# Optimization experiments

Measured on AMD Instinct MI355X. Metric: run time of the kernel, lower is better.

## Reference

```python
import jax, jax.numpy as jnp
from jax import lax
import numpy as np

D_MODEL, D_STATE, EXPAND, D_CONV = 1024, 16, 2, 4
D_INNER = EXPAND * D_MODEL
B, L = 4, 2048


def setup_inputs() -> dict:
    key = jax.random.key(0)
    ks = jax.random.split(key, 12)
    def xavier(k, shape):
        fan_in, fan_out = shape[1], shape[0]
        lim = float(np.sqrt(6.0 / (fan_in + fan_out)))
        return jax.random.uniform(k, shape, jnp.float32, -lim, lim)
    inp = {}
    inp['x'] = jax.random.normal(ks[0], (B, L, D_MODEL), jnp.float32)
    inp['W_left'] = xavier(ks[1], (D_INNER, D_MODEL))
    inp['conv_w'] = jax.random.normal(ks[2], (D_INNER, 1, D_CONV), jnp.float32) * (1.0 / np.sqrt(D_CONV))
    inp['conv_b'] = jax.random.normal(ks[3], (D_INNER,), jnp.float32) * 0.01
    inp['W_delta'] = jax.random.normal(ks[4], (D_INNER, D_INNER), jnp.float32) * (1.0 / np.sqrt(D_INNER))
    inp['b_delta'] = jnp.zeros((D_INNER,), jnp.float32)
    inp['W_B'] = jax.random.normal(ks[5], (D_STATE, D_INNER), jnp.float32) * (1.0 / np.sqrt(D_INNER))
    inp['W_C'] = jax.random.normal(ks[6], (D_STATE, D_INNER), jnp.float32) * (1.0 / np.sqrt(D_INNER))
    inp['A_log'] = jnp.log(jnp.arange(1, D_STATE + 1, dtype=jnp.float32))
    inp['W_right'] = xavier(ks[7], (D_INNER, D_MODEL))
    inp['ln_g'] = jnp.ones((D_INNER,), jnp.float32)
    inp['ln_b'] = jnp.zeros((D_INNER,), jnp.float32)
    inp['W_out'] = xavier(ks[8], (D_MODEL, D_INNER))
    return inp


def _ssm(xl, W_delta, b_delta, W_B, W_C, A_log):
    # xl: [b, l, d_inner]
    b, l, d_inner = xl.shape
    A = -jax.nn.softplus(A_log)  # [d_state]
    delta = jnp.clip(jax.nn.softplus(xl @ W_delta.T + b_delta), 1e-4, 10.0)
    Bm = xl @ W_B.T  # [b, l, d_state]
    Cm = xl @ W_C.T  # [b, l, d_state]

    def step(h, inp):
        d_t, x_t, B_t, C_t = inp  # [b,d_inner], [b,d_inner], [b,N], [b,N]
        A_bar = jnp.exp(d_t[:, :, None] * A)            # [b, d_inner, N]
        h = A_bar * h + (d_t * x_t)[:, :, None] * B_t[:, None, :]
        y_t = jnp.einsum('bdn,bn->bd', h, C_t)
        return h, y_t

    h0 = jnp.zeros((b, d_inner, A_log.shape[0]), xl.dtype)
    xs = (jnp.swapaxes(delta, 0, 1), jnp.swapaxes(xl, 0, 1),
          jnp.swapaxes(Bm, 0, 1), jnp.swapaxes(Cm, 0, 1))
    _, ys = lax.scan(step, h0, xs)  # ys: [l, b, d_inner]
    return jnp.swapaxes(ys, 0, 1)


def reference(x, W_left, conv_w, conv_b, W_delta, b_delta, W_B, W_C, A_log,
              W_right, ln_g, ln_b, W_out):
    d_conv = conv_w.shape[-1]
    # left branch: linear -> causal depthwise conv1d -> silu
    left = x @ W_left.T                          # [b, l, d_inner]
    left_ncw = jnp.swapaxes(left, 1, 2)          # [b, d_inner, l]
    left_ncw = jnp.pad(left_ncw, ((0, 0), (0, 0), (d_conv - 1, 0)))
    left_ncw = lax.conv_general_dilated(
        left_ncw, conv_w, window_strides=(1,), padding='VALID',
        feature_group_count=conv_w.shape[0]) + conv_b[None, :, None]
    left = jax.nn.silu(jnp.swapaxes(left_ncw, 1, 2))
    # selective scan
    ssm_out = _ssm(left, W_delta, b_delta, W_B, W_C, A_log)
    # right gate (eval mode: dropout off)
    gate = jax.nn.silu(x @ W_right.T)
    out = ssm_out * gate
    # layernorm over d_inner
    mu = jnp.mean(out, axis=-1, keepdims=True)
    var = jnp.mean(jnp.square(out - mu), axis=-1, keepdims=True)
    out = (out - mu) * lax.rsqrt(var + 1e-5) * ln_g + ln_b
    return out @ W_out.T
```

## Files before the change

### kernel.cpp

```cpp
#include <hip/hip_runtime.h>
#include <cstddef>

#define LL 2048
#define TOK 8192
#define DM 1024
#define DI 2048
#define NS 16

typedef _Float16 half_t;
typedef __attribute__((ext_vector_type(8))) _Float16 f16x8;
typedef __attribute__((ext_vector_type(4))) _Float16 f16x4;
typedef __attribute__((ext_vector_type(4))) float f32x4;

__device__ __forceinline__ float softplus_f(float x) {
  return fmaxf(x, 0.f) + log1pf(__expf(-fabsf(x)));
}
__device__ __forceinline__ float silu_f(float x) {
  return x / (1.f + __expf(-x));
}
__device__ __forceinline__ void gload_lds16(const void* g, void* l) {
  __builtin_amdgcn_global_load_lds((const __attribute__((address_space(1))) void*)g,
                                   (__attribute__((address_space(3))) void*)l, 16, 0, 0);
}
#define DPP_ADD(v, ctrl) \
  ((v) + __int_as_float(__builtin_amdgcn_update_dpp(0, __float_as_int(v), (ctrl), 0xf, 0xf, true)))

__device__ float g_buf[120881152];

__global__ __launch_bounds__(256) void f2h_k(const float* __restrict__ in,
                                             half_t* __restrict__ out, int n4) {
  const int i = blockIdx.x * 256 + threadIdx.x;
  if (i >= n4) return;
  const float4 v = ((const float4*)in)[i];
  f16x4 o;
  o[0] = (half_t)v.x; o[1] = (half_t)v.y; o[2] = (half_t)v.z; o[3] = (half_t)v.w;
  ((f16x4*)out)[i] = o;
}

__global__ __launch_bounds__(256) void zh_k(half_t* __restrict__ out, int n4) {
  const int i = blockIdx.x * 256 + threadIdx.x;
  if (i >= n4) return;
  f16x4 o;
  o[0] = (half_t)0.f; o[1] = (half_t)0.f; o[2] = (half_t)0.f; o[3] = (half_t)0.f;
  ((f16x4*)out)[i] = o;
}

template <int ACT>
__global__ __launch_bounds__(256) void gemm_mfma(const half_t* __restrict__ A,
                                                 const half_t* __restrict__ W,
                                                 const float* __restrict__ bias,
                                                 float* __restrict__ C,
                                                 int M, int N, int K) {
  __shared__ half_t lA[4096];
  __shared__ half_t lB[4096];
  const int tid = threadIdx.x;
  const int bm0 = blockIdx.y * 128, bn0 = blockIdx.x * 128;
  const int lane = tid & 63, wave = tid >> 6;
  const int q = lane >> 4, mr = lane & 15;
  const int wm = (wave >> 1) * 64, wn = (wave & 1) * 64;
  const int flat0 = tid, flat1 = tid + 256;
  const int kc0 = flat0 >> 7, r0 = flat0 & 127;
  const int kc1 = flat1 >> 7, r1 = flat1 & 127;

  f32x4 acc[4][4];
#pragma unroll
  for (int i = 0; i < 4; ++i)
#pragma unroll
    for (int j = 0; j < 4; ++j) acc[i][j] = (f32x4){0.f, 0.f, 0.f, 0.f};

  for (int k0 = 0; k0 < K; k0 += 32) {
    gload_lds16(A + (size_t)(bm0 + r0) * K + k0 + kc0 * 8, lA + (size_t)flat0 * 8);
    gload_lds16(A + (size_t)(bm0 + r1) * K + k0 + kc1 * 8, lA + (size_t)flat1 * 8);
    gload_lds16(W + (size_t)(bn0 + r0) * K + k0 + kc0 * 8, lB + (size_t)flat0 * 8);
    gload_lds16(W + (size_t)(bn0 + r1) * K + k0 + kc1 * 8, lB + (size_t)flat1 * 8);
    __syncthreads();
    f16x8 af[4], bg[4];
#pragma unroll
    for (int t = 0; t < 4; ++t) {
      af[t] = *(const f16x8*)(lA + ((q << 10) + ((wm + t * 16 + mr) << 3)));
      bg[t] = *(const f16x8*)(lB + ((q << 10) + ((wn + t * 16 + mr) << 3)));
    }
#pragma unroll
    for (int i = 0; i < 4; ++i)
#pragma unroll
      for (int j = 0; j < 4; ++j)
        acc[i][j] = __builtin_amdgcn_mfma_f32_16x16x32_f16(af[i], bg[j], acc[i][j], 0, 0, 0);
    __syncthreads();
  }

#pragma unroll
  for (int i = 0; i < 4; ++i) {
#pragma unroll
    for (int j = 0; j < 4; ++j) {
      const int col = bn0 + wn + j * 16 + mr;
      const float bv = bias ? bias[col] : 0.f;
#pragma unroll
      for (int r = 0; r < 4; ++r) {
        const int row = bm0 + wm + i * 16 + q * 4 + r;
        float v = acc[i][j][r] + bv;
        if (ACT == 1) v = silu_f(v);
        C[(size_t)row * N + col] = v;
      }
    }
  }
}

__global__ __launch_bounds__(256) void gemm_mfma_lg(const half_t* __restrict__ A,
                                                    const half_t* __restrict__ W,
                                                    float* __restrict__ left,
                                                    half_t* __restrict__ gateh) {
  __shared__ half_t lA[4096];
  __shared__ half_t lB[4096];
  const int tid = threadIdx.x;
  const int bm0 = blockIdx.y * 128, bn0 = blockIdx.x * 128;
  const int K = DM;
  const int lane = tid & 63, wave = tid >> 6;
  const int q = lane >> 4, mr = lane & 15;
  const int wm = (wave >> 1) * 64, wn = (wave & 1) * 64;
  const int flat1 = tid + 256;
  const int kc0 = tid >> 7, r0 = tid & 127;
  const int kc1 = flat1 >> 7, r1 = flat1 & 127;

  f32x4 acc[4][4];
#pragma unroll
  for (int i = 0; i < 4; ++i)
#pragma unroll
    for (int j = 0; j < 4; ++j) acc[i][j] = (f32x4){0.f, 0.f, 0.f, 0.f};

  for (int k0 = 0; k0 < K; k0 += 32) {
    gload_lds16(A + (size_t)(bm0 + r0) * K + k0 + kc0 * 8, lA + (size_t)tid * 8);
    gload_lds16(A + (size_t)(bm0 + r1) * K + k0 + kc1 * 8, lA + (size_t)flat1 * 8);
    gload_lds16(W + (size_t)(bn0 + r0) * K + k0 + kc0 * 8, lB + (size_t)tid * 8);
    gload_lds16(W + (size_t)(bn0 + r1) * K + k0 + kc1 * 8, lB + (size_t)flat1 * 8);
    __syncthreads();
    f16x8 af[4], bg[4];
#pragma unroll
    for (int t = 0; t < 4; ++t) {
      af[t] = *(const f16x8*)(lA + ((q << 10) + ((wm + t * 16 + mr) << 3)));
      bg[t] = *(const f16x8*)(lB + ((q << 10) + ((wn + t * 16 + mr) << 3)));
    }
#pragma unroll
    for (int i = 0; i < 4; ++i)
#pragma unroll
      for (int j = 0; j < 4; ++j)
        acc[i][j] = __builtin_amdgcn_mfma_f32_16x16x32_f16(af[i], bg[j], acc[i][j], 0, 0, 0);
    __syncthreads();
  }

  const int is_gate = (bn0 >= DI);
  const int cb = bn0 - (is_gate ? DI : 0);
  if (!is_gate) {
#pragma unroll
    for (int i = 0; i < 4; ++i)
#pragma unroll
      for (int j = 0; j < 4; ++j) {
        const int col = cb + wn + j * 16 + mr;
#pragma unroll
        for (int r = 0; r < 4; ++r) {
          const int row = bm0 + wm + i * 16 + q * 4 + r;
          left[(size_t)row * DI + col] = acc[i][j][r];
        }
      }
  } else {
#pragma unroll
    for (int i = 0; i < 4; ++i)
#pragma unroll
      for (int j = 0; j < 4; ++j) {
        const int col = cb + wn + j * 16 + mr;
#pragma unroll
        for (int r = 0; r < 4; ++r) {
          const int row = bm0 + wm + i * 16 + q * 4 + r;
          gateh[(size_t)row * DI + col] = (half_t)silu_f(acc[i][j][r]);
        }
      }
  }
}

__global__ __launch_bounds__(512, 4) void gemm_delta_bc(const half_t* __restrict__ A,
                                                        const half_t* __restrict__ W,
                                                        const float* __restrict__ bias,
                                                        half_t* __restrict__ dlth,
                                                        float* __restrict__ bcout) {
  __shared__ half_t lA[8192];
  __shared__ half_t lB[4096];
  const int tid = threadIdx.x;
  const int bm0 = blockIdx.y * 256, bn0 = blockIdx.x * 128;
  const int K = DI;
  const int lane = tid & 63, wave = tid >> 6;
  const int q = lane >> 4, mr = lane & 15;
  const int wm = (wave >> 1) * 64, wn = (wave & 1) * 64;
  const int aflat1 = tid + 512;
  const int akc0 = tid >> 8, ar0 = tid & 255;
  const int akc1 = aflat1 >> 8, ar1 = aflat1 & 255;
  const int wkc = tid >> 7, wr = tid & 127;

  f32x4 acc[4][4];
#pragma unroll
  for (int i = 0; i < 4; ++i)
#pragma unroll
    for (int j = 0; j < 4; ++j) acc[i][j] = (f32x4){0.f, 0.f, 0.f, 0.f};

  for (int k0 = 0; k0 < K; k0 += 32) {
    gload_lds16(A + (size_t)(bm0 + ar0) * K + k0 + akc0 * 8, lA + (size_t)tid * 8);
    gload_lds16(A + (size_t)(bm0 + ar1) * K + k0 + akc1 * 8, lA + (size_t)aflat1 * 8);
    gload_lds16(W + (size_t)(bn0 + wr) * K + k0 + wkc * 8, lB + (size_t)tid * 8);
    __syncthreads();
    f16x8 ah[4], bg[4];
#pragma unroll
    for (int t = 0; t < 4; ++t) {
      const int ao = (q << 11) + ((wm + t * 16 + mr) << 3);
      const int bo = (q << 10) + ((wn + t * 16 + mr) << 3);
      ah[t] = *(const f16x8*)(lA + ao);
      bg[t] = *(const f16x8*)(lB + bo);
    }
    __builtin_amdgcn_s_setprio(1);
#pragma unroll
    for (int i = 0; i < 4; ++i)
#pragma unroll
      for (int j = 0; j < 4; ++j)
        acc[i][j] = __builtin_amdgcn_mfma_f32_16x16x32_f16(ah[i], bg[j], acc[i][j], 0, 0, 0);
    __builtin_amdgcn_s_setprio(0);
    __syncthreads();
  }

  if (bn0 < DI) {
#pragma unroll
    for (int i = 0; i < 4; ++i) {
#pragma unroll
      for (int j = 0; j < 4; ++j) {
        const int col = bn0 + wn + j * 16 + mr;
        const float bv = bias[col];
#pragma unroll
        for (int r = 0; r < 4; ++r) {
          const int row = bm0 + wm + i * 16 + q * 4 + r;
          float v = softplus_f(acc[i][j][r] + bv);
          v = fminf(fmaxf(v, 1e-4f), 10.f);
          dlth[(size_t)row * DI + col] = (half_t)v;
        }
      }
    }
  } else {
#pragma unroll
    for (int i = 0; i < 4; ++i) {
#pragma unroll
      for (int j = 0; j < 4; ++j) {
        const int c = wn + j * 16 + mr;
        if (c < 32) {
          const int slot = (c < 16) ? (2 * c) : (2 * (c - 16) + 1);
#pragma unroll
          for (int r = 0; r < 4; ++r) {
            const int row = bm0 + wm + i * 16 + q * 4 + r;
            bcout[(size_t)row * 32 + slot] = acc[i][j][r];
          }
        }
      }
    }
  }
}

__global__ __launch_bounds__(256) void conv_silu_k(const float* __restrict__ left,
                                                   const float* __restrict__ cw,
                                                   const float* __restrict__ cb,
                                                   half_t* __restrict__ xch) {
  const int idx = blockIdx.x * 256 + threadIdx.x;
  const int d = idx & (DI - 1);
  const int bt = idx >> 11;
  const int t = bt & (LL - 1);
  const float4 wv = *(const float4*)(cw + (size_t)d * 4);
  float acc = cb[d];
  const size_t base = (size_t)idx;
  if (t >= 3) {
    acc += left[base - 3 * DI] * wv.x + left[base - 2 * DI] * wv.y +
           left[base - DI] * wv.z + left[base] * wv.w;
  } else {
    acc += left[base] * wv.w;
    if (t >= 1) acc += left[base - DI] * wv.z;
    if (t >= 2) acc += left[base - 2 * DI] * wv.y;
  }
  xch[base] = (half_t)silu_f(acc);
}

#define ST 32
__global__ __launch_bounds__(256) void scan_k(const half_t* __restrict__ dlth,
                                              const half_t* __restrict__ xch,
                                              const half_t* __restrict__ gateh,
                                              const float* __restrict__ bcp,
                                              const float* __restrict__ A_log,
                                              float* __restrict__ y) {
  __shared__ float dx2[16 * 68];
  __shared__ float bcs[ST * 32];
  __shared__ float ys[ST * 16];
  const int tid = threadIdx.x;
  const int b  = blockIdx.x >> 7;
  const int d0 = (blockIdx.x & 127) << 4;
  const int n  = tid & 15;
  const int ch = tid >> 4;
  const float An = -softplus_f(A_log[n]);

  const int t_a = tid >> 4, c_a = tid & 15;
  const int t_b = t_a + 16;

  float h = 0.f;
  const size_t batch_base = (size_t)b * LL * DI + d0;
  const size_t batch_bc   = (size_t)b * LL * 32;

  size_t rb_cur = batch_base;
  float g0, g1;
  {
    const size_t ra = rb_cur + (size_t)t_a * DI + c_a;
    const size_t rbx = rb_cur + (size_t)t_b * DI + c_a;
    const float d0v = (float)dlth[ra], x0v = (float)xch[ra];
    const float d1v = (float)dlth[rbx], x1v = (float)xch[rbx];
    g0 = (float)gateh[ra]; g1 = (float)gateh[rbx];
    const float2 b0 = *(const float2*)&bcp[batch_bc + (size_t)t_a * 32 + 2 * c_a];
    const float2 b1 = *(const float2*)&bcp[batch_bc + (size_t)t_b * 32 + 2 * c_a];
    *(float2*)&dx2[c_a * 68 + t_a * 2] = make_float2(d0v, x0v);
    *(float2*)&dx2[c_a * 68 + t_b * 2] = make_float2(d1v, x1v);
    *(float2*)&bcs[t_a * 32 + 2 * c_a] = b0;
    *(float2*)&bcs[t_b * 32 + 2 * c_a] = b1;
  }
  __syncthreads();

  for (int it = 0; it < LL / ST; ++it) {
    float nd0, nx0, ng0, nd1, nx1, ng1;
    float2 nb0, nb1;
    const size_t rb_nxt = batch_base + (size_t)(it + 1) * ST * DI;
    if (it + 1 < LL / ST) {
      const size_t ra = rb_nxt + (size_t)t_a * DI + c_a;
      const size_t rbx = rb_nxt + (size_t)t_b * DI + c_a;
      nd0 = (float)dlth[ra]; nx0 = (float)xch[ra]; ng0 = (float)gateh[ra];
      nd1 = (float)dlth[rbx]; nx1 = (float)xch[rbx]; ng1 = (float)gateh[rbx];
      const size_t bcb = batch_bc + (size_t)(it + 1) * ST * 32;
      nb0 = *(const float2*)&bcp[bcb + (size_t)t_a * 32 + 2 * c_a];
      nb1 = *(const float2*)&bcp[bcb + (size_t)t_b * 32 + 2 * c_a];
    }

    const float* dxp = &dx2[ch * 68];
#pragma unroll
    for (int tt = 0; tt < ST; tt += 2) {
      const float4 v = *(const float4*)&dxp[tt * 2];
      const float2 bc0 = *(const float2*)&bcs[tt * 32 + 2 * n];
      const float2 bc1 = *(const float2*)&bcs[(tt + 1) * 32 + 2 * n];
      float ab = __expf(v.x * An);
      h = fmaf(ab, h, v.x * v.y * bc0.x);
      float p = h * bc0.y;
      p = DPP_ADD(p, 0x111); p = DPP_ADD(p, 0x112);
      p = DPP_ADD(p, 0x114); p = DPP_ADD(p, 0x118);
      if (n == 15) ys[tt * 16 + ch] = p;
      ab = __expf(v.z * An);
      h = fmaf(ab, h, v.z * v.w * bc1.x);
      p = h * bc1.y;
      p = DPP_ADD(p, 0x111); p = DPP_ADD(p, 0x112);
      p = DPP_ADD(p, 0x114); p = DPP_ADD(p, 0x118);
      if (n == 15) ys[(tt + 1) * 16 + ch] = p;
    }
    __syncthreads();

    if (it + 1 < LL / ST) {
      *(float2*)&dx2[c_a * 68 + t_a * 2] = make_float2(nd0, nx0);
      *(float2*)&dx2[c_a * 68 + t_b * 2] = make_float2(nd1, nx1);
      *(float2*)&bcs[t_a * 32 + 2 * c_a] = nb0;
      *(float2*)&bcs[t_b * 32 + 2 * c_a] = nb1;
    }
    y[rb_cur + (size_t)t_a * DI + c_a] = ys[t_a * 16 + c_a] * g0;
    y[rb_cur + (size_t)t_b * DI + c_a] = ys[t_b * 16 + c_a] * g1;
    g0 = ng0; g1 = ng1;
    rb_cur = rb_nxt;
    __syncthreads();
  }
}

__global__ __launch_bounds__(256) void ln_k(const float* __restrict__ y,
                                            const float* __restrict__ gam,
                                            const float* __restrict__ bet,
                                            half_t* __restrict__ outn) {
  const int row = blockIdx.x;
  const int tid = threadIdx.x;
  const float* yr = y + (size_t)row * DI;
  const float4 v0 = ((const float4*)yr)[tid];
  const float4 v1 = ((const float4*)yr)[tid + 256];
  float s = v0.x + v0.y + v0.z + v0.w + v1.x + v1.y + v1.z + v1.w;
  float q = v0.x * v0.x + v0.y * v0.y + v0.z * v0.z + v0.w * v0.w +
            v1.x * v1.x + v1.y * v1.y + v1.z * v1.z + v1.w * v1.w;
  for (int off = 32; off > 0; off >>= 1) {
    s += __shfl_down(s, off);
    q += __shfl_down(q, off);
  }
  __shared__ float sred[4], qred[4];
  const int wid = tid >> 6;
  if ((tid & 63) == 0) { sred[wid] = s; qred[wid] = q; }
  __syncthreads();
  s = sred[0] + sred[1] + sred[2] + sred[3];
  q = qred[0] + qred[1] + qred[2] + qred[3];
  const float mu = s * (1.f / DI);
  const float rs = rsqrtf(q * (1.f / DI) - mu * mu + 1e-5f);
  half_t* orow = outn + (size_t)row * DI;
  const int c0 = tid * 4, c1 = (tid + 256) * 4;
  f16x4 o;
  o[0] = (half_t)((v0.x - mu) * rs * gam[c0 + 0] + bet[c0 + 0]);
  o[1] = (half_t)((v0.y - mu) * rs * gam[c0 + 1] + bet[c0 + 1]);
  o[2] = (half_t)((v0.z - mu) * rs * gam[c0 + 2] + bet[c0 + 2]);
  o[3] = (half_t)((v0.w - mu) * rs * gam[c0 + 3] + bet[c0 + 3]);
  ((f16x4*)orow)[tid] = o;
  o[0] = (half_t)((v1.x - mu) * rs * gam[c1 + 0] + bet[c1 + 0]);
  o[1] = (half_t)((v1.y - mu) * rs * gam[c1 + 1] + bet[c1 + 1]);
  o[2] = (half_t)((v1.z - mu) * rs * gam[c1 + 2] + bet[c1 + 2]);
  o[3] = (half_t)((v1.w - mu) * rs * gam[c1 + 3] + bet[c1 + 3]);
  ((f16x4*)orow)[tid + 256] = o;
}

extern "C" void kernel_launch(void* const* d_in, const int* in_sizes, int n_in,
                              void* d_out, int out_size, void* d_ws, size_t ws_size,
                              hipStream_t stream) {
  const float* x       = (const float*)d_in[0];
  const float* W_left  = (const float*)d_in[1];
  const float* conv_w  = (const float*)d_in[2];
  const float* conv_b  = (const float*)d_in[3];
  const float* W_delta = (const float*)d_in[4];
  const float* b_delta = (const float*)d_in[5];
  const float* W_B     = (const float*)d_in[6];
  const float* W_C     = (const float*)d_in[7];
  const float* A_log   = (const float*)d_in[8];
  const float* W_right = (const float*)d_in[9];
  const float* ln_g    = (const float*)d_in[10];
  const float* ln_b    = (const float*)d_in[11];
  const float* W_out   = (const float*)d_in[12];

  float* buf = nullptr;
  hipGetSymbolAddress((void**)&buf, HIP_SYMBOL(g_buf));
  half_t* xh    = (half_t*)(buf + 0);
  half_t* wlgh  = (half_t*)(buf + 4194304);
  half_t* wrh   = (half_t*)(buf + 5242880);
  half_t* wdf   = (half_t*)(buf + 6291456);
  half_t* woh   = (half_t*)(buf + 10485760);
  float* left   = buf + 11534336;
  half_t* xch   = (half_t*)(buf + 45088768);
  half_t* dlth  = (half_t*)(buf + 61865984);
  half_t* gateh = (half_t*)(buf + 78643200);
  float* yv     = buf + 95420416;
  half_t* nrmh  = (half_t*)(buf + 112197632);
  float* bc     = buf + 120586240;

  f2h_k<<<8192, 256, 0, stream>>>(x, xh, TOK * DM / 4);
  f2h_k<<<2048, 256, 0, stream>>>(W_left, wlgh, DI * DM / 4);
  f2h_k<<<2048, 256, 0, stream>>>(W_right, wrh, DI * DM / 4);
  f2h_k<<<2048, 256, 0, stream>>>(W_out, woh, DM * DI / 4);
  f2h_k<<<4096, 256, 0, stream>>>(W_delta, wdf, DI * DI / 4);
  f2h_k<<<32, 256, 0, stream>>>(W_B, wdf + (size_t)DI * DI, NS * DI / 4);
  f2h_k<<<32, 256, 0, stream>>>(W_C, wdf + (size_t)(DI + NS) * DI, NS * DI / 4);
  zh_k<<<192, 256, 0, stream>>>(wdf + (size_t)(DI + 2 * NS) * DI, 96 * DI / 4);

  gemm_mfma_lg<<<dim3(2 * DI / 128, TOK / 128), 256, 0, stream>>>(xh, wlgh, left, gateh);
  conv_silu_k<<<TOK * DI / 256, 256, 0, stream>>>(left, conv_w, conv_b, xch);
  gemm_delta_bc<<<dim3(17, TOK / 256), 512, 0, stream>>>(xch, wdf, b_delta, dlth, bc);
  scan_k<<<512, 256, 0, stream>>>(dlth, xch, gateh, bc, A_log, yv);
  ln_k<<<TOK, 256, 0, stream>>>(yv, ln_g, ln_b, nrmh);
  gemm_mfma<0><<<dim3(DM / 128, TOK / 128), 256, 0, stream>>>(nrmh, woh, nullptr, (float*)d_out, TOK, DM, DI);
}
```

Baseline: 970.5 us.

## Split-K the delta/BC and output GEMMs with atomic fp32 accumulation

The delta/B/C projection GEMM is split along K into two halves and the output GEMM into four K-slices. Partial results are combined with float atomicAdd into zeroed fp32 buffers, and separate finalize kernels apply bias, softplus and clamp to delta and reorder B/C. The aim is more blocks in flight to fill the GPU's compute units. The cost is extra zeroing passes, an fp32 round trip for delta, atomic traffic, and a summation order that is no longer deterministic.

```diff
diff --git a/kernel.cpp b/kernel.cpp
--- a/kernel.cpp
+++ b/kernel.cpp
@@ -45,64 +45,10 @@
   ((f16x4*)out)[i] = o;
 }
 
-template <int ACT>
-__global__ __launch_bounds__(256) void gemm_mfma(const half_t* __restrict__ A,
-                                                 const half_t* __restrict__ W,
-                                                 const float* __restrict__ bias,
-                                                 float* __restrict__ C,
-                                                 int M, int N, int K) {
-  __shared__ half_t lA[4096];
-  __shared__ half_t lB[4096];
-  const int tid = threadIdx.x;
-  const int bm0 = blockIdx.y * 128, bn0 = blockIdx.x * 128;
-  const int lane = tid & 63, wave = tid >> 6;
-  const int q = lane >> 4, mr = lane & 15;
-  const int wm = (wave >> 1) * 64, wn = (wave & 1) * 64;
-  const int flat0 = tid, flat1 = tid + 256;
-  const int kc0 = flat0 >> 7, r0 = flat0 & 127;
-  const int kc1 = flat1 >> 7, r1 = flat1 & 127;
-
-  f32x4 acc[4][4];
-#pragma unroll
-  for (int i = 0; i < 4; ++i)
-#pragma unroll
-    for (int j = 0; j < 4; ++j) acc[i][j] = (f32x4){0.f, 0.f, 0.f, 0.f};
-
-  for (int k0 = 0; k0 < K; k0 += 32) {
-    gload_lds16(A + (size_t)(bm0 + r0) * K + k0 + kc0 * 8, lA + (size_t)flat0 * 8);
-    gload_lds16(A + (size_t)(bm0 + r1) * K + k0 + kc1 * 8, lA + (size_t)flat1 * 8);
-    gload_lds16(W + (size_t)(bn0 + r0) * K + k0 + kc0 * 8, lB + (size_t)flat0 * 8);
-    gload_lds16(W + (size_t)(bn0 + r1) * K + k0 + kc1 * 8, lB + (size_t)flat1 * 8);
-    __syncthreads();
-    f16x8 af[4], bg[4];
-#pragma unroll
-    for (int t = 0; t < 4; ++t) {
-      af[t] = *(const f16x8*)(lA + ((q << 10) + ((wm + t * 16 + mr) << 3)));
-      bg[t] = *(const f16x8*)(lB + ((q << 10) + ((wn + t * 16 + mr) << 3)));
-    }
-#pragma unroll
-    for (int i = 0; i < 4; ++i)
-#pragma unroll
-      for (int j = 0; j < 4; ++j)
-        acc[i][j] = __builtin_amdgcn_mfma_f32_16x16x32_f16(af[i], bg[j], acc[i][j], 0, 0, 0);
-    __syncthreads();
-  }
-
-#pragma unroll
-  for (int i = 0; i < 4; ++i) {
-#pragma unroll
-    for (int j = 0; j < 4; ++j) {
-      const int col = bn0 + wn + j * 16 + mr;
-      const float bv = bias ? bias[col] : 0.f;
-#pragma unroll
-      for (int r = 0; r < 4; ++r) {
-        const int row = bm0 + wm + i * 16 + q * 4 + r;
-        float v = acc[i][j][r] + bv;
-        if (ACT == 1) v = silu_f(v);
-        C[(size_t)row * N + col] = v;
-      }
-    }
-  }
+__global__ __launch_bounds__(256) void zero_f32(float* __restrict__ p, int n4) {
+  const int i = blockIdx.x * 256 + threadIdx.x;
+  if (i >= n4) return;
+  ((float4*)p)[i] = make_float4(0.f, 0.f, 0.f, 0.f);
 }
 
 __global__ __launch_bounds__(256) void gemm_mfma_lg(const half_t* __restrict__ A,
@@ -176,16 +122,16 @@
   }
 }
 
-__global__ __launch_bounds__(512, 4) void gemm_delta_bc(const half_t* __restrict__ A,
+__global__ __launch_bounds__(512, 4) void gemm_delta_sk(const half_t* __restrict__ A,
                                                         const half_t* __restrict__ W,
-                                                        const float* __restrict__ bias,
-                                                        half_t* __restrict__ dlth,
-                                                        float* __restrict__ bcout) {
+                                                        float* __restrict__ dlt32,
+                                                        float* __restrict__ bc32) {
   __shared__ half_t lA[8192];
   __shared__ half_t lB[4096];
   const int tid = threadIdx.x;
   const int bm0 = blockIdx.y * 256, bn0 = blockIdx.x * 128;
   const int K = DI;
+  const int kz0 = blockIdx.z * (DI / 2);
   const int lane = tid & 63, wave = tid >> 6;
   const int q = lane >> 4, mr = lane & 15;
   const int wm = (wave >> 1) * 64, wn = (wave & 1) * 64;
@@ -200,7 +146,7 @@
 #pragma unroll
     for (int j = 0; j < 4; ++j) acc[i][j] = (f32x4){0.f, 0.f, 0.f, 0.f};
 
-  for (int k0 = 0; k0 < K; k0 += 32) {
+  for (int k0 = kz0; k0 < kz0 + DI / 2; k0 += 32) {
     gload_lds16(A + (size_t)(bm0 + ar0) * K + k0 + akc0 * 8, lA + (size_t)tid * 8);
     gload_lds16(A + (size_t)(bm0 + ar1) * K + k0 + akc1 * 8, lA + (size_t)aflat1 * 8);
     gload_lds16(W + (size_t)(bn0 + wr) * K + k0 + wkc * 8, lB + (size_t)tid * 8);
@@ -229,13 +175,10 @@
 #pragma unroll
       for (int j = 0; j < 4; ++j) {
         const int col = bn0 + wn + j * 16 + mr;
-        const float bv = bias[col];
 #pragma unroll
         for (int r = 0; r < 4; ++r) {
           const int row = bm0 + wm + i * 16 + q * 4 + r;
-          float v = softplus_f(acc[i][j][r] + bv);
-          v = fminf(fmaxf(v, 1e-4f), 10.f);
-          dlth[(size_t)row * DI + col] = (half_t)v;
+          atomicAdd(&dlt32[(size_t)row * DI + col], acc[i][j][r]);
         }
       }
     }
@@ -245,14 +188,90 @@
 #pragma unroll
       for (int j = 0; j < 4; ++j) {
         const int c = wn + j * 16 + mr;
-        if (c < 32) {
-          const int slot = (c < 16) ? (2 * c) : (2 * (c - 16) + 1);
-#pragma unroll
-          for (int r = 0; r < 4; ++r) {
-            const int row = bm0 + wm + i * 16 + q * 4 + r;
-            bcout[(size_t)row * 32 + slot] = acc[i][j][r];
-          }
+#pragma unroll
+        for (int r = 0; r < 4; ++r) {
+          const int row = bm0 + wm + i * 16 + q * 4 + r;
+          atomicAdd(&bc32[(size_t)row * 128 + c], acc[i][j][r]);
         }
+      }
+    }
+  }
+}
+
+__global__ __launch_bounds__(256) void delta_fin(const float* __restrict__ dlt32,
+                                                 const float* __restrict__ bias,
+                                                 half_t* __restrict__ dlth) {
+  const int i = blockIdx.x * 256 + threadIdx.x;
+  const float4 v = ((const float4*)dlt32)[i];
+  const int col4 = (i * 4) & (DI - 1);
+  const float4 bv = *(const float4*)&bias[col4];
+  f16x4 o;
+  o[0] = (half_t)fminf(fmaxf(softplus_f(v.x + bv.x), 1e-4f), 10.f);
+  o[1] = (half_t)fminf(fmaxf(softplus_f(v.y + bv.y), 1e-4f), 10.f);
+  o[2] = (half_t)fminf(fmaxf(softplus_f(v.z + bv.z), 1e-4f), 10.f);
+  o[3] = (half_t)fminf(fmaxf(softplus_f(v.w + bv.w), 1e-4f), 10.f);
+  ((f16x4*)dlth)[i] = o;
+}
+
+__global__ __launch_bounds__(256) void bc_fin(const float* __restrict__ bc32,
+                                              float* __restrict__ bc) {
+  const int i = blockIdx.x * 256 + threadIdx.x;
+  const int row = i >> 5, c = i & 31;
+  const int slot = (c < 16) ? (2 * c) : (2 * (c - 16) + 1);
+  bc[(size_t)row * 32 + slot] = bc32[(size_t)row * 128 + c];
+}
+
+__global__ __launch_bounds__(256) void gemm_out_sk(const half_t* __restrict__ A,
+                                                   const half_t* __restrict__ W,
+                                                   float* __restrict__ C) {
+  __shared__ half_t lA[4096];
+  __shared__ half_t lB[4096];
+  const int tid = threadIdx.x;
+  const int bm0 = blockIdx.y * 128, bn0 = blockIdx.x * 128;
+  const int K = DI, N = DM;
+  const int kz0 = blockIdx.z * (DI / 4);
+  const int lane = tid & 63, wave = tid >> 6;
+  const int q = lane >> 4, mr = lane & 15;
+  const int wm = (wave >> 1) * 64, wn = (wave & 1) * 64;
+  const int flat1 = tid + 256;
+  const int kc0 = tid >> 7, r0 = tid & 127;
+  const int kc1 = flat1 >> 7, r1 = flat1 & 127;
+
+  f32x4 acc[4][4];
+#pragma unroll
+  for (int i = 0; i < 4; ++i)
+#pragma unroll
+    for (int j = 0; j < 4; ++j) acc[i][j] = (f32x4){0.f, 0.f, 0.f, 0.f};
+
+  for (int k0 = kz0; k0 < kz0 + DI / 4; k0 += 32) {
+    gload_lds16(A + (size_t)(bm0 + r0) * K + k0 + kc0 * 8, lA + (size_t)tid * 8);
+    gload_lds16(A + (size_t)(bm0 + r1) * K + k0 + kc1 * 8, lA + (size_t)flat1 * 8);
+    gload_lds16(W + (size_t)(bn0 + r0) * K + k0 + kc0 * 8, lB + (size_t)tid * 8);
+    gload_lds16(W + (size_t)(bn0 + r1) * K + k0 + kc1 * 8, lB + (size_t)flat1 * 8);
+    __syncthreads();
+    f16x8 af[4], bg[4];
+#pragma unroll
+    for (int t = 0; t < 4; ++t) {
+      af[t] = *(const f16x8*)(lA + ((q << 10) + ((wm + t * 16 + mr) << 3)));
+      bg[t] = *(const f16x8*)(lB + ((q << 10) + ((wn + t * 16 + mr) << 3)));
+    }
+#pragma unroll
+    for (int i = 0; i < 4; ++i)
+#pragma unroll
+      for (int j = 0; j < 4; ++j)
+        acc[i][j] = __builtin_amdgcn_mfma_f32_16x16x32_f16(af[i], bg[j], acc[i][j], 0, 0, 0);
+    __syncthreads();
+  }
+
+#pragma unroll
+  for (int i = 0; i < 4; ++i) {
+#pragma unroll
+    for (int j = 0; j < 4; ++j) {
+      const int col = bn0 + wn + j * 16 + mr;
+#pragma unroll
+      for (int r = 0; r < 4; ++r) {
+        const int row = bm0 + wm + i * 16 + q * 4 + r;
+        atomicAdd(&C[(size_t)row * N + col], acc[i][j][r]);
       }
     }
   }
@@ -434,12 +453,18 @@
   half_t* wdf   = (half_t*)(buf + 6291456);
   half_t* woh   = (half_t*)(buf + 10485760);
   float* left   = buf + 11534336;
+  float* dlt32  = buf + 28311552;
   half_t* xch   = (half_t*)(buf + 45088768);
+  float* bc32   = buf + 53477376;
   half_t* dlth  = (half_t*)(buf + 61865984);
   half_t* gateh = (half_t*)(buf + 78643200);
   float* yv     = buf + 95420416;
   half_t* nrmh  = (half_t*)(buf + 112197632);
   float* bc     = buf + 120586240;
+
+  zero_f32<<<16384, 256, 0, stream>>>(dlt32, TOK * DI / 4);
+  zero_f32<<<1024, 256, 0, stream>>>(bc32, TOK * 128 / 4);
+  zero_f32<<<8192, 256, 0, stream>>>((float*)d_out, TOK * DM / 4);
 
   f2h_k<<<8192, 256, 0, stream>>>(x, xh, TOK * DM / 4);
   f2h_k<<<2048, 256, 0, stream>>>(W_left, wlgh, DI * DM / 4);
@@ -452,8 +477,10 @@
 
   gemm_mfma_lg<<<dim3(2 * DI / 128, TOK / 128), 256, 0, stream>>>(xh, wlgh, left, gateh);
   conv_silu_k<<<TOK * DI / 256, 256, 0, stream>>>(left, conv_w, conv_b, xch);
-  gemm_delta_bc<<<dim3(17, TOK / 256), 512, 0, stream>>>(xch, wdf, b_delta, dlth, bc);
+  gemm_delta_sk<<<dim3(17, TOK / 256, 2), 512, 0, stream>>>(xch, wdf, dlt32, bc32);
+  delta_fin<<<TOK * DI / 1024, 256, 0, stream>>>(dlt32, b_delta, dlth);
+  bc_fin<<<TOK * 32 / 256, 256, 0, stream>>>(bc32, bc);
   scan_k<<<512, 256, 0, stream>>>(dlth, xch, gateh, bc, A_log, yv);
   ln_k<<<TOK, 256, 0, stream>>>(yv, ln_g, ln_b, nrmh);
-  gemm_mfma<0><<<dim3(DM / 128, TOK / 128), 256, 0, stream>>>(nrmh, woh, nullptr, (float*)d_out, TOK, DM, DI);
-}
+  gemm_out_sk<<<dim3(DM / 128, TOK / 128, 4), 256, 0, stream>>>(nrmh, woh, (float*)d_out);
+}
```

After: 1.233 ms. +27.1%, slower.
